# Performance work log

Hardware: AMD Instinct MI355X
Metric: run time of the kernel (lower is better)

Reference implementation:

```python
import jax, jax.numpy as jnp
import numpy as np

D_STATE = 16
D_CONV = 4
DT_RANK = 16  # ceil(d_model/16) = ceil(256/16)
N_LAYERS = 2
EPS = 1e-5


def _layernorm(x, g, b):
    m = jnp.mean(x, -1, keepdims=True)
    v = jnp.var(x, -1, keepdims=True)
    return (x - m) * jax.lax.rsqrt(v + EPS) * g + b


def _causal_conv(x, w, b):
    # x [B,L,D], depthwise causal conv, w [D,K], b [D]
    K = w.shape[1]
    L = x.shape[1]
    xp = jnp.pad(x, ((0, 0), (K - 1, 0), (0, 0)))
    y = sum(xp[:, k:k + L, :] * w[:, k] for k in range(K))
    return y + b


def _selective_scan(u, dt, A, Bm, Cm, D_skip):
    # u, dt [B,L,d]; A [d,n]; Bm, Cm [B,L,n]; D_skip [d]
    def step(h, inp):
        dt_t, B_t, C_t, u_t = inp  # [B,d],[B,n],[B,n],[B,d]
        dA = jnp.exp(dt_t[:, :, None] * A)                      # [B,d,n]
        h = dA * h + dt_t[:, :, None] * B_t[:, None, :] * u_t[:, :, None]
        y = jnp.einsum('bdn,bn->bd', h, C_t)
        return h, y

    Bsz, L, d = u.shape
    h0 = jnp.zeros((Bsz, d, A.shape[1]), u.dtype)
    xs = (dt.transpose(1, 0, 2), Bm.transpose(1, 0, 2),
          Cm.transpose(1, 0, 2), u.transpose(1, 0, 2))
    _, ys = jax.lax.scan(step, h0, xs)                          # [L,B,d]
    return ys.transpose(1, 0, 2) + u * D_skip


def _mamba_block(x, Wip, cw, cb, Wxp, Wdt, bdt, Alog, Dp, Wout):
    xz = x @ Wip                                                # [B,L,2*d_inner]
    d_inner = Wip.shape[1] // 2
    xc, z = xz[..., :d_inner], xz[..., d_inner:]
    xc = jax.nn.silu(_causal_conv(xc, cw, cb))
    xdbl = xc @ Wxp                                             # [B,L,dt_rank+2n]
    dt = jax.nn.softplus(xdbl[..., :DT_RANK] @ Wdt + bdt)
    Bm = xdbl[..., DT_RANK:DT_RANK + D_STATE]
    Cm = xdbl[..., DT_RANK + D_STATE:]
    A = -jnp.exp(Alog)
    y = _selective_scan(xc, dt, A, Bm, Cm, Dp)
    y = y * jax.nn.silu(z)
    return y @ Wout


def reference(z_t, W_in, b_in, ln_g, ln_b, W_inproj, conv_w, conv_b, W_xproj,
              W_dt, b_dt, A_log, D_skip, W_out, W_outp, b_outp, lno_g, lno_b):
    x = z_t @ W_in + b_in                                       # [B,L,d_model]
    for i in range(N_LAYERS):
        res = x
        xn = _layernorm(x, ln_g[i], ln_b[i])
        x = res + _mamba_block(xn, W_inproj[i], conv_w[i], conv_b[i],
                               W_xproj[i], W_dt[i], b_dt[i], A_log[i],
                               D_skip[i], W_out[i])  # dropout is identity in eval
    u = x @ W_outp + b_outp
    return _layernorm(u, lno_g, lno_b)


def setup_inputs() -> dict:
    key = jax.random.key(0)
    B, L = 16, 2048
    d_input, d_model, d_output, d_inner = 1088, 256, 64, 512
    n = N_LAYERS
    ks = jax.random.split(key, 10)

    def rn(k, shape, fan):
        return jax.random.normal(k, shape, jnp.float32) / np.float32(np.sqrt(fan))

    A_init = jnp.log(jnp.arange(1, D_STATE + 1, dtype=jnp.float32))
    return {
        'z_t': jax.random.normal(ks[0], (B, L, d_input), jnp.float32),
        'W_in': rn(ks[1], (d_input, d_model), d_input),
        'b_in': jnp.zeros((d_model,), jnp.float32),
        'ln_g': jnp.ones((n, d_model), jnp.float32),
        'ln_b': jnp.zeros((n, d_model), jnp.float32),
        'W_inproj': rn(ks[2], (n, d_model, 2 * d_inner), d_model),
        'conv_w': rn(ks[3], (n, d_inner, D_CONV), D_CONV),
        'conv_b': jnp.zeros((n, d_inner), jnp.float32),
        'W_xproj': rn(ks[4], (n, d_inner, DT_RANK + 2 * D_STATE), d_inner),
        'W_dt': rn(ks[5], (n, DT_RANK, d_inner), DT_RANK),
        'b_dt': jnp.full((n, d_inner), -4.6, jnp.float32),  # softplus ~ 0.01
        'A_log': jnp.broadcast_to(A_init, (n, d_inner, D_STATE)) + 0.0,
        'D_skip': jnp.ones((n, d_inner), jnp.float32),
        'W_out': rn(ks[6], (n, d_inner, d_model), d_inner),
        'W_outp': rn(ks[7], (d_model, d_output), d_model),
        'b_outp': jnp.zeros((d_output,), jnp.float32),
        'lno_g': jnp.ones((d_output,), jnp.float32),
        'lno_b': jnp.zeros((d_output,), jnp.float32),
    }
```

## Files before the change

kernel.cpp:

```cpp
#include <hip/hip_runtime.h>
#include <hip/hip_bf16.h>
#include <math.h>
#include <stdint.h>

#define L_SEQ 2048
#define BATCH 16
#define NROWS (BATCH * L_SEQ)
#define DMODEL 256
#define DINNER 512
#define C_CH 32
#define T_CH 64
#define LOG2E 1.4426950408889634f

typedef __attribute__((ext_vector_type(8))) __bf16 bf16x8;
typedef __attribute__((ext_vector_type(4))) float f32x4;
typedef __attribute__((ext_vector_type(8))) unsigned short u16x8;
typedef __attribute__((address_space(1))) const uint32_t gu32;
typedef __attribute__((address_space(3))) uint32_t lu32;

#if __has_builtin(__builtin_amdgcn_exp2f)
#define EXP2F __builtin_amdgcn_exp2f
#else
#define EXP2F exp2f
#endif

__device__ __forceinline__ float sigmoidf_(float x) { return 1.f / (1.f + __expf(-x)); }

__device__ __forceinline__ unsigned short f2bf(float f) {
    union { float f; uint32_t u; } v; v.f = f;
    uint32_t r = v.u + 0x7FFF + ((v.u >> 16) & 1);
    return (unsigned short)(r >> 16);
}
__device__ __forceinline__ float bf2f(unsigned short h) {
    union { uint32_t u; float f; } v; v.u = ((uint32_t)h) << 16;
    return v.f;
}

__device__ __forceinline__ void gld16(const void* g, void* l) {
    __builtin_amdgcn_global_load_lds((gu32*)g, (lu32*)l, 16, 0, 0);
}

template <int N> __device__ __forceinline__ void waitv() {
    if constexpr (N == 0)       asm volatile("s_waitcnt vmcnt(0)" ::: "memory");
    else if constexpr (N == 3)  asm volatile("s_waitcnt vmcnt(3)" ::: "memory");
    else if constexpr (N == 4)  asm volatile("s_waitcnt vmcnt(4)" ::: "memory");
    else if constexpr (N == 6)  asm volatile("s_waitcnt vmcnt(6)" ::: "memory");
    else if constexpr (N == 8)  asm volatile("s_waitcnt vmcnt(8)" ::: "memory");
    else if constexpr (N == 16) asm volatile("s_waitcnt vmcnt(16)" ::: "memory");
}

__global__ __launch_bounds__(256) void wtrans_all(
    const float* __restrict__ W_in, const float* __restrict__ W_inpr,
    const float* __restrict__ W_out, const float* __restrict__ W_xproj,
    const float* __restrict__ W_outp,
    unsigned short* __restrict__ WinT, unsigned short* __restrict__ WipT,
    unsigned short* __restrict__ WoutT, unsigned short* __restrict__ WxpT,
    unsigned short* __restrict__ WopT)
{
    const int bid = blockIdx.x, tid = threadIdx.x;
    if (bid < 1088) {
        int idx = bid * 256 + tid;
        int n = idx / 1088, k = idx % 1088;
        WinT[idx] = f2bf(W_in[(size_t)k * 256 + n]);
    } else if (bid < 3136) {
        int l = (bid - 1088) >> 10;
        int idx = ((bid - 1088) & 1023) * 256 + tid;
        int n = idx >> 8, k = idx & 255;
        WipT[(size_t)l * 262144 + idx] = f2bf(W_inpr[(size_t)l * 262144 + (size_t)k * 1024 + n]);
    } else if (bid < 4160) {
        int l = (bid - 3136) >> 9;
        int idx = ((bid - 3136) & 511) * 256 + tid;
        int n = idx >> 9, k = idx & 511;
        WoutT[(size_t)l * 131072 + idx] = f2bf(W_out[(size_t)l * 131072 + (size_t)k * 256 + n]);
    } else if (bid < 4672) {
        int l = (bid - 4160) >> 8;
        int idx = ((bid - 4160) & 255) * 256 + tid;
        int n = idx >> 9, k = idx & 511;
        WxpT[(size_t)l * 65536 + idx] =
            (n < 48) ? f2bf(W_xproj[(size_t)l * (512 * 48) + (size_t)k * 48 + n]) : (unsigned short)0;
    } else {
        int idx = (bid - 4672) * 256 + tid;
        int n = idx >> 8, k = idx & 255;
        WopT[idx] = (n < 64) ? f2bf(W_outp[(size_t)k * 64 + n]) : (unsigned short)0;
    }
}

template <int TM, int TN, int BK, bool A_F32, bool HAS_BIAS, bool HAS_RES, bool OUT_BF16, bool LN64OUT>
__global__ __launch_bounds__(256) void gemm_bf16(
    const void* __restrict__ Aptr, const unsigned short* __restrict__ Bt,
    const float* __restrict__ bias, const float* __restrict__ res,
    void* __restrict__ Cout, int M, int N, int K, int Nout,
    const float* __restrict__ lng, const float* __restrict__ lnb)
{
    constexpr int MR = TM / 32;
    constexpr int NR = TN / 32;
    constexpr int EWA = A_F32 ? 4 : 2;
    constexpr int RBA = BK * EWA;
    constexpr int RBB = BK * 2;
    constexpr int ABYTES = TM * RBA;
    constexpr int BBYTES = TN * RBB;
    constexpr int OPSA = ABYTES / 4096;
    constexpr int OPSB = BBYTES / 4096;
    constexpr int VOPS = OPSA + OPSB;
    constexpr bool SWZA = (RBA >= 128);
    constexpr bool SWZB = (RBB >= 128);
    constexpr int KK = BK / 32;
    __shared__ __align__(16) char Alds[2][ABYTES];
    __shared__ __align__(16) char Blds[2][BBYTES];
    const int tid = threadIdx.x;
    const int w = tid >> 6, lane = tid & 63;

    const int nwg = gridDim.x;
    const int q = nwg >> 3;
    const int wg = (blockIdx.x & 7) * q + (blockIdx.x >> 3);
    const int nx = N / TN;
    const int bm = (wg / nx) * TM, bn = (wg % nx) * TN;

    const int wr = (w >> 1) * (TM / 2), wc = (w & 1) * (TN / 2);
    const int fr = lane & 15, fq = lane >> 4;
    const size_t KbB = (size_t)K * 2;
    const size_t KbA = (size_t)K * EWA;

    const char* Ab = (const char*)Aptr;
    const char* Bb = (const char*)Bt;
    const int lds0 = w * 1024;

    f32x4 acc[MR][NR];
#pragma unroll
    for (int m = 0; m < MR; m++)
#pragma unroll
        for (int n = 0; n < NR; n++) acc[m][n] = (f32x4){0.f, 0.f, 0.f, 0.f};

    auto stageA = [&](int buf, int k0) {
        char* lA = Alds[buf];
#pragma unroll
        for (int i = 0; i < OPSA; i++) {
            const int o = i * 4096 + tid * 16;
            const int row = o / RBA;
            int col = o % RBA;
            if constexpr (SWZA) col ^= (row & 7) << 4;
            gld16(Ab + (size_t)(bm + row) * KbA + (size_t)k0 * EWA + col,
                  lA + i * 4096 + lds0);
        }
    };
    auto stageB = [&](int buf, int k0) {
        char* lB = Blds[buf];
#pragma unroll
        for (int i = 0; i < OPSB; i++) {
            const int o = i * 4096 + tid * 16;
            const int row = o / RBB;
            int col = o % RBB;
            if constexpr (SWZB) col ^= (row & 7) << 4;
            gld16(Bb + (size_t)(bn + row) * KbB + (size_t)k0 * 2 + col,
                  lB + i * 4096 + lds0);
        }
    };
    auto compute = [&](int buf) {
        const char* lA = Alds[buf];
        const char* lB = Blds[buf];
#pragma unroll
        for (int kk = 0; kk < KK; kk++) {
            bf16x8 af[MR], bg[NR];
#pragma unroll
            for (int m = 0; m < MR; m++) {
                const int row = wr + m * 16 + fr;
                const int sw = SWZA ? ((row & 7) << 4) : 0;
                if constexpr (A_F32) {
                    const int b0 = row * RBA + kk * 128 + fq * 32;
                    float4 x0 = *(const float4*)(lA + (b0 ^ sw));
                    float4 x1 = *(const float4*)(lA + ((b0 + 16) ^ sw));
                    bf16x8 a;
                    a[0]=(__bf16)x0.x; a[1]=(__bf16)x0.y; a[2]=(__bf16)x0.z; a[3]=(__bf16)x0.w;
                    a[4]=(__bf16)x1.x; a[5]=(__bf16)x1.y; a[6]=(__bf16)x1.z; a[7]=(__bf16)x1.w;
                    af[m] = a;
                } else {
                    const int c = kk * 64 + fq * 16;
                    af[m] = *(const bf16x8*)(lA + row * RBA + (c ^ sw));
                }
            }
#pragma unroll
            for (int n = 0; n < NR; n++) {
                const int row = wc + n * 16 + fr;
                const int sw = SWZB ? ((row & 7) << 4) : 0;
                const int c = kk * 64 + fq * 16;
                bg[n] = *(const bf16x8*)(lB + row * RBB + (c ^ sw));
            }
#pragma unroll
            for (int m = 0; m < MR; m++)
#pragma unroll
                for (int n = 0; n < NR; n++)
                    acc[m][n] = __builtin_amdgcn_mfma_f32_16x16x32_bf16(af[m], bg[n], acc[m][n], 0, 0, 0);
        }
    };

    const int NT = K / BK;

    stageA(0, 0); stageB(0, 0);
    asm volatile("s_waitcnt vmcnt(0) lgkmcnt(0)" ::: "memory");
    __builtin_amdgcn_s_barrier();
    __builtin_amdgcn_sched_barrier(0);

    for (int kt = 0; kt < NT; ++kt) {
        const int cur = kt & 1;
        const bool has_next = (kt + 1 < NT);
        if (has_next) {
            const int k0 = (kt + 1) * BK;
            stageA(cur ^ 1, k0); stageB(cur ^ 1, k0);
            waitv<VOPS>();
        } else {
            waitv<0>();
        }
        __builtin_amdgcn_s_barrier();
        __builtin_amdgcn_sched_barrier(0);

        compute(cur);

        asm volatile("s_waitcnt lgkmcnt(0)" ::: "memory");
        __builtin_amdgcn_s_barrier();
        __builtin_amdgcn_sched_barrier(0);
    }

    if constexpr (LN64OUT) {
        if (wc == 0) {
#pragma unroll
            for (int m = 0; m < MR; m++) {
#pragma unroll
                for (int r = 0; r < 4; r++) {
                    float v[NR]; float s = 0.f, sq = 0.f;
#pragma unroll
                    for (int n = 0; n < NR; n++) {
                        v[n] = acc[m][n][r] + bias[n * 16 + fr];
                        s += v[n]; sq += v[n] * v[n];
                    }
#pragma unroll
                    for (int off = 8; off; off >>= 1) { s += __shfl_xor(s, off); sq += __shfl_xor(sq, off); }
                    float mean = s * (1.f / 64.f);
                    float var = sq * (1.f / 64.f) - mean * mean;
                    float rs = rsqrtf(var + 1e-5f);
                    int row = bm + wr + m * 16 + fq * 4 + r;
#pragma unroll
                    for (int n = 0; n < NR; n++) {
                        int col = n * 16 + fr;
                        ((float*)Cout)[(size_t)row * 64 + col] = (v[n] - mean) * rs * lng[col] + lnb[col];
                    }
                }
            }
        }
    } else {
#pragma unroll
        for (int m = 0; m < MR; m++) {
#pragma unroll
            for (int n = 0; n < NR; n++) {
                int col = bn + wc + n * 16 + fr;
                if (col < Nout) {
#pragma unroll
                    for (int r = 0; r < 4; r++) {
                        int row = bm + wr + m * 16 + fq * 4 + r;
                        float v = acc[m][n][r];
                        if (HAS_BIAS) v += bias[col];
                        if (HAS_RES)  v += res[(size_t)row * Nout + col];
                        if (OUT_BF16) ((unsigned short*)Cout)[(size_t)row * Nout + col] = f2bf(v);
                        else          ((float*)Cout)[(size_t)row * Nout + col] = v;
                    }
                }
            }
        }
    }
}

__global__ __launch_bounds__(256) void ln256(
    const float* __restrict__ x, const float* __restrict__ g,
    const float* __restrict__ b, unsigned short* __restrict__ out)
{
    int lane = threadIdx.x & 63, wid = threadIdx.x >> 6;
    size_t r = (size_t)blockIdx.x * 4 + wid;
    const float4 v = *(const float4*)&x[r * 256 + lane * 4];
    float s = v.x + v.y + v.z + v.w;
    float sq = v.x * v.x + v.y * v.y + v.z * v.z + v.w * v.w;
#pragma unroll
    for (int off = 32; off; off >>= 1) { s += __shfl_xor(s, off); sq += __shfl_xor(sq, off); }
    float mean = s * (1.f / 256.f);
    float var = sq * (1.f / 256.f) - mean * mean;
    float rs = rsqrtf(var + 1e-5f);
    float4 gv = *(const float4*)&g[lane * 4];
    float4 bv = *(const float4*)&b[lane * 4];
    ushort4 o;
    o.x = f2bf((v.x - mean) * rs * gv.x + bv.x);
    o.y = f2bf((v.y - mean) * rs * gv.y + bv.y);
    o.z = f2bf((v.z - mean) * rs * gv.z + bv.z);
    o.w = f2bf((v.w - mean) * rs * gv.w + bv.w);
    *(ushort4*)&out[r * 256 + lane * 4] = o;
}

__global__ __launch_bounds__(256) void conv_silu8(
    const unsigned short* __restrict__ xz, const float* __restrict__ w,
    const float* __restrict__ cb, unsigned short* __restrict__ xc)
{
    int idx = blockIdx.x * 256 + threadIdx.x;
    int d8 = (idx & 63) << 3;
    int l  = (idx >> 6) & 2047;
    int b  = idx >> 17;
    const unsigned short* base = xz + ((size_t)b * L_SEQ + l) * 1024 + d8;
    u16x8 t0 = {0,0,0,0,0,0,0,0}, t1 = t0, t2 = t0;
    u16x8 t3 = *(const u16x8*)base;
    if (l >= 1) t2 = *(const u16x8*)(base - 1024);
    if (l >= 2) t1 = *(const u16x8*)(base - 2048);
    if (l >= 3) t0 = *(const u16x8*)(base - 3072);
    u16x8 o;
#pragma unroll
    for (int j = 0; j < 8; j++) {
        float4 wv = *(const float4*)&w[(d8 + j) * 4];
        float acc = cb[d8 + j];
        acc = fmaf(bf2f(t0[j]), wv.x, acc);
        acc = fmaf(bf2f(t1[j]), wv.y, acc);
        acc = fmaf(bf2f(t2[j]), wv.z, acc);
        acc = fmaf(bf2f(t3[j]), wv.w, acc);
        o[j] = f2bf(acc * sigmoidf_(acc));
    }
    *(u16x8*)&xc[((size_t)b * L_SEQ + l) * 512 + d8] = o;
}

__global__ __launch_bounds__(256) void scan_pass1(
    const unsigned short* __restrict__ xc, const float* __restrict__ xdbl,
    const float* __restrict__ Wdt, const float* __restrict__ bdt,
    const float* __restrict__ Alog,
    float* __restrict__ Tbuf, float* __restrict__ Sbuf)
{
    __shared__ float xs[T_CH][32];
    int idx = blockIdx.x * 256 + threadIdx.x;
    int d = idx & 511;
    int c = (idx >> 9) & (C_CH - 1);
    int b = idx >> 14;
    size_t r0 = (size_t)b * L_SEQ + (size_t)c * T_CH;
#pragma unroll
    for (int ii = 0; ii < 2; ii++) {
        int i = threadIdx.x + ii * 256, row = i >> 3, qq = i & 7;
        *(float4*)&xs[row][qq * 4] = *(const float4*)&xdbl[(r0 + row) * 48 + qq * 4];
    }
    __syncthreads();

    float wdt[16];
#pragma unroll
    for (int j = 0; j < 16; j++) wdt[j] = Wdt[j * 512 + d];
    const float bd = bdt[d];

    float a[16], a2[16], S[16];
#pragma unroll
    for (int n = 0; n < 16; n++) a[n] = -__expf(Alog[d * 16 + n]);
#pragma unroll
    for (int n = 0; n < 16; n++) a2[n] = a[n] * LOG2E;
#pragma unroll
    for (int n = 0; n < 16; n++) S[n] = 0.f;
    bool pow_ok = true;
#pragma unroll
    for (int n = 1; n < 16; n++)
        pow_ok = pow_ok && (fabsf(a[n] - (n + 1) * a[0]) <= 1e-3f * (n + 1) * fabsf(a[0]));
    const float a0l2 = a[0] * LOG2E;
    float Tsum = 0.f;

    if (pow_ok) {
        for (int t = 0; t < T_CH; t++) {
            float dtr = bd;
#pragma unroll
            for (int j = 0; j < 16; j++) dtr = fmaf(xs[t][j], wdt[j], dtr);
            float dtv = (dtr > 20.f) ? dtr : __logf(1.f + __expf(dtr));
            float u = bf2f(xc[(r0 + t) * 512 + d]);
            float dtu = dtv * u;
            Tsum += dtv;
            float e1 = EXP2F(dtv * a0l2), e2 = e1 * e1;
            S[0] = fmaf(e1, S[0], dtu * xs[t][16]);
            S[1] = fmaf(e2, S[1], dtu * xs[t][17]);
            float pm2 = e1, pm1 = e2;
#pragma unroll
            for (int n = 2; n < 16; n++) {
                float cur = pm2 * e2;
                S[n] = fmaf(cur, S[n], dtu * xs[t][16 + n]);
                pm2 = pm1; pm1 = cur;
            }
        }
    } else {
        for (int t = 0; t < T_CH; t++) {
            float dtr = bd;
#pragma unroll
            for (int j = 0; j < 16; j++) dtr = fmaf(xs[t][j], wdt[j], dtr);
            float dtv = (dtr > 20.f) ? dtr : __logf(1.f + __expf(dtr));
            float u = bf2f(xc[(r0 + t) * 512 + d]);
            float dtu = dtv * u;
            Tsum += dtv;
#pragma unroll
            for (int n = 0; n < 16; n++) {
                float dA = EXP2F(dtv * a2[n]);
                S[n] = fmaf(dA, S[n], dtu * xs[t][16 + n]);
            }
        }
    }
    Tbuf[idx] = Tsum;
    size_t o = (size_t)idx * 16;
#pragma unroll
    for (int qq = 0; qq < 4; qq++)
        *(float4*)&Sbuf[o + qq * 4] = make_float4(S[qq*4], S[qq*4+1], S[qq*4+2], S[qq*4+3]);
}

__global__ __launch_bounds__(256) void scan_pass2(
    const float* __restrict__ Tbuf, const float* __restrict__ Alog,
    float* __restrict__ Sbuf)
{
    int g = blockIdx.x * 256 + threadIdx.x;
    int nd = g & 8191;
    int b = g >> 13;
    int d = nd >> 4, n = nd & 15;
    const float a2 = -__expf(Alog[d * 16 + n]) * LOG2E;
    float H = 0.f;
    for (int c = 0; c < C_CH; c++) {
        size_t base = (size_t)(b * C_CH + c);
        float T = Tbuf[base * 512 + d];
        float P = EXP2F(T * a2);
        size_t idx = base * 8192 + nd;
        float S = Sbuf[idx];
        float Hn = fmaf(P, H, S);
        Sbuf[idx] = H;
        H = Hn;
    }
}

__global__ __launch_bounds__(256) void scan_pass3(
    const unsigned short* __restrict__ xcin, const unsigned short* __restrict__ xz,
    const float* __restrict__ xdbl, const float* __restrict__ Wdt,
    const float* __restrict__ bdt, const float* __restrict__ Alog,
    const float* __restrict__ Dsk, const float* __restrict__ Sbuf,
    unsigned short* __restrict__ y)
{
    __shared__ float xs[T_CH][48];
    int idx = blockIdx.x * 256 + threadIdx.x;
    int d = idx & 511;
    int c = (idx >> 9) & (C_CH - 1);
    int b = idx >> 14;
    size_t r0 = (size_t)b * L_SEQ + (size_t)c * T_CH;
#pragma unroll
    for (int ii = 0; ii < 3; ii++) {
        int i = threadIdx.x + ii * 256, row = i / 12, qq = i % 12;
        *(float4*)&xs[row][qq * 4] = *(const float4*)&xdbl[(r0 + row) * 48 + qq * 4];
    }
    __syncthreads();

    float wdt[16];
#pragma unroll
    for (int j = 0; j < 16; j++) wdt[j] = Wdt[j * 512 + d];
    const float bd = bdt[d];

    float a[16], a2[16], h[16];
#pragma unroll
    for (int n = 0; n < 16; n++) a[n] = -__expf(Alog[d * 16 + n]);
#pragma unroll
    for (int n = 0; n < 16; n++) a2[n] = a[n] * LOG2E;
    {
        size_t o = (size_t)idx * 16;
#pragma unroll
        for (int qq = 0; qq < 4; qq++) {
            float4 v = *(const float4*)&Sbuf[o + qq * 4];
            h[qq*4] = v.x; h[qq*4+1] = v.y; h[qq*4+2] = v.z; h[qq*4+3] = v.w;
        }
    }
    bool pow_ok = true;
#pragma unroll
    for (int n = 1; n < 16; n++)
        pow_ok = pow_ok && (fabsf(a[n] - (n + 1) * a[0]) <= 1e-3f * (n + 1) * fabsf(a[0]));
    const float a0l2 = a[0] * LOG2E;
    const float Dv = Dsk[d];

    if (pow_ok) {
        for (int t = 0; t < T_CH; t++) {
            size_t ridx = (r0 + t) * 512 + d;
            float dtr = bd;
#pragma unroll
            for (int j = 0; j < 16; j++) dtr = fmaf(xs[t][j], wdt[j], dtr);
            float dtv = (dtr > 20.f) ? dtr : __logf(1.f + __expf(dtr));
            float u = bf2f(xcin[ridx]);
            float dtu = dtv * u;
            float e1 = EXP2F(dtv * a0l2), e2 = e1 * e1;
            float yv = 0.f;
            h[0] = fmaf(e1, h[0], dtu * xs[t][16]);  yv = fmaf(h[0], xs[t][32], yv);
            h[1] = fmaf(e2, h[1], dtu * xs[t][17]);  yv = fmaf(h[1], xs[t][33], yv);
            float pm2 = e1, pm1 = e2;
#pragma unroll
            for (int n = 2; n < 16; n++) {
                float cur = pm2 * e2;
                h[n] = fmaf(cur, h[n], dtu * xs[t][16 + n]);
                yv = fmaf(h[n], xs[t][32 + n], yv);
                pm2 = pm1; pm1 = cur;
            }
            yv = fmaf(u, Dv, yv);
            float z = bf2f(xz[(r0 + t) * 1024 + 512 + d]);
            y[ridx] = f2bf(yv * z * sigmoidf_(z));
        }
    } else {
        for (int t = 0; t < T_CH; t++) {
            size_t ridx = (r0 + t) * 512 + d;
            float dtr = bd;
#pragma unroll
            for (int j = 0; j < 16; j++) dtr = fmaf(xs[t][j], wdt[j], dtr);
            float dtv = (dtr > 20.f) ? dtr : __logf(1.f + __expf(dtr));
            float u = bf2f(xcin[ridx]);
            float dtu = dtv * u;
            float yv = 0.f;
#pragma unroll
            for (int n = 0; n < 16; n++) {
                float dA = EXP2F(dtv * a2[n]);
                h[n] = fmaf(dA, h[n], dtu * xs[t][16 + n]);
                yv = fmaf(h[n], xs[t][32 + n], yv);
            }
            yv = fmaf(u, Dv, yv);
            float z = bf2f(xz[(r0 + t) * 1024 + 512 + d]);
            y[ridx] = f2bf(yv * z * sigmoidf_(z));
        }
    }
}

extern "C" void kernel_launch(void* const* d_in, const int* in_sizes, int n_in,
                              void* d_out, int out_size, void* d_ws, size_t ws_size,
                              hipStream_t stream)
{
    const float* z_t     = (const float*)d_in[0];
    const float* W_in    = (const float*)d_in[1];
    const float* b_in    = (const float*)d_in[2];
    const float* ln_g    = (const float*)d_in[3];
    const float* ln_b    = (const float*)d_in[4];
    const float* W_inpr  = (const float*)d_in[5];
    const float* conv_w  = (const float*)d_in[6];
    const float* conv_b  = (const float*)d_in[7];
    const float* W_xproj = (const float*)d_in[8];
    const float* W_dt    = (const float*)d_in[9];
    const float* b_dt    = (const float*)d_in[10];
    const float* A_log   = (const float*)d_in[11];
    const float* D_skip  = (const float*)d_in[12];
    const float* W_out   = (const float*)d_in[13];
    const float* W_outp  = (const float*)d_in[14];
    const float* b_outp  = (const float*)d_in[15];
    const float* lno_g   = (const float*)d_in[16];
    const float* lno_b   = (const float*)d_in[17];
    float* out           = (float*)d_out;

    char* p = (char*)d_ws;
    float*          x    = (float*)p;          p += (size_t)NROWS * DMODEL * 4;
    unsigned short* xn   = (unsigned short*)p; p += (size_t)NROWS * DMODEL * 2;
    unsigned short* xc   = (unsigned short*)p; p += (size_t)NROWS * DINNER * 2;
    unsigned short* xz   = (unsigned short*)p; p += (size_t)NROWS * 1024 * 2;
    float*          xdbl = (float*)p;          p += (size_t)NROWS * 48 * 4;
    float*          Pregion = (float*)p;       p += (size_t)BATCH * C_CH * DINNER * 16 * 4;
    float*          Sbuf = (float*)p;          p += (size_t)BATCH * C_CH * DINNER * 16 * 4;
    unsigned short* WinT  = (unsigned short*)p; p += (size_t)256 * 1088 * 2;
    unsigned short* WipT  = (unsigned short*)p; p += (size_t)2 * 1024 * 256 * 2;
    unsigned short* WoutT = (unsigned short*)p; p += (size_t)2 * 256 * 512 * 2;
    unsigned short* WxpT  = (unsigned short*)p; p += (size_t)2 * 128 * 512 * 2;
    unsigned short* WopT  = (unsigned short*)p; p += (size_t)128 * 256 * 2;
    float* Tbuf = Pregion;

    wtrans_all<<<4800, 256, 0, stream>>>(W_in, W_inpr, W_out, W_xproj, W_outp,
                                         WinT, WipT, WoutT, WxpT, WopT);

    gemm_bf16<64, 128, 64, true, true, false, false, false><<<(NROWS / 64) * (256 / 128), 256, 0, stream>>>(
        z_t, WinT, b_in, nullptr, x, NROWS, 256, 1088, 256, nullptr, nullptr);

    for (int layer = 0; layer < 2; ++layer) {
        ln256<<<NROWS / 4, 256, 0, stream>>>(x, ln_g + layer * 256, ln_b + layer * 256, xn);
        gemm_bf16<128, 128, 64, false, false, false, true, false><<<(NROWS / 128) * (1024 / 128), 256, 0, stream>>>(
            xn, WipT + (size_t)layer * 1024 * 256, nullptr, nullptr, xz, NROWS, 1024, 256, 1024, nullptr, nullptr);
        conv_silu8<<<NROWS * 64 / 256, 256, 0, stream>>>(
            xz, conv_w + layer * 512 * 4, conv_b + layer * 512, xc);
        gemm_bf16<64, 128, 64, false, false, false, false, false><<<(NROWS / 64) * (128 / 128), 256, 0, stream>>>(
            xc, WxpT + (size_t)layer * 128 * 512, nullptr, nullptr, xdbl, NROWS, 128, 512, 48, nullptr, nullptr);

        const float* Al_l  = A_log + layer * 512 * 16;
        const float* Wdt_l = W_dt + layer * 16 * 512;
        const float* bdt_l = b_dt + layer * 512;
        scan_pass1<<<BATCH * C_CH * DINNER / 256, 256, 0, stream>>>(
            xc, xdbl, Wdt_l, bdt_l, Al_l, Tbuf, Sbuf);
        scan_pass2<<<BATCH * DINNER * 16 / 256, 256, 0, stream>>>(Tbuf, Al_l, Sbuf);
        scan_pass3<<<BATCH * C_CH * DINNER / 256, 256, 0, stream>>>(
            xc, xz, xdbl, Wdt_l, bdt_l, Al_l, D_skip + layer * 512, Sbuf, xc);

        if (layer == 0) {
            gemm_bf16<64, 128, 64, false, false, true, false, false><<<(NROWS / 64) * (256 / 128), 256, 0, stream>>>(
                xc, WoutT, nullptr, x, x, NROWS, 256, 512, 256, nullptr, nullptr);
        } else {
            gemm_bf16<64, 128, 64, false, false, true, true, false><<<(NROWS / 64) * (256 / 128), 256, 0, stream>>>(
                xc, WoutT + (size_t)256 * 512, nullptr, x, xn, NROWS, 256, 512, 256, nullptr, nullptr);
        }
    }

    gemm_bf16<64, 128, 64, false, true, false, false, true><<<(NROWS / 64) * (128 / 128), 256, 0, stream>>>(
        xn, WopT, b_outp, nullptr, out, NROWS, 128, 256, 64, lno_g, lno_b);
}
```

Before: 526.6 us.

## Fuse LayerNorm into full-row GEMM epilogues for input and out projections

Removes the standalone ln256 kernel by widening the input-projection GEMM and the layer-0 output-projection GEMM to cover all 256 output columns per block (TN=256, BK=32). Their epilogues now compute per-row mean and variance through shuffles plus a cross-warp LDS reduction, then write both the fp32 residual and the bf16 normalized activations. This saves a full read of x and a separate launch per layer. In exchange, those GEMMs use different tiling with fewer blocks and a smaller K step, which may hurt occupancy or pipelining.

```diff
diff --git a/kernel.cpp b/kernel.cpp
--- a/kernel.cpp
+++ b/kernel.cpp
@@ -44,8 +44,10 @@
     if constexpr (N == 0)       asm volatile("s_waitcnt vmcnt(0)" ::: "memory");
     else if constexpr (N == 3)  asm volatile("s_waitcnt vmcnt(3)" ::: "memory");
     else if constexpr (N == 4)  asm volatile("s_waitcnt vmcnt(4)" ::: "memory");
+    else if constexpr (N == 5)  asm volatile("s_waitcnt vmcnt(5)" ::: "memory");
     else if constexpr (N == 6)  asm volatile("s_waitcnt vmcnt(6)" ::: "memory");
     else if constexpr (N == 8)  asm volatile("s_waitcnt vmcnt(8)" ::: "memory");
+    else if constexpr (N == 10) asm volatile("s_waitcnt vmcnt(10)" ::: "memory");
     else if constexpr (N == 16) asm volatile("s_waitcnt vmcnt(16)" ::: "memory");
 }
 
@@ -85,12 +87,14 @@
     }
 }
 
-template <int TM, int TN, int BK, bool A_F32, bool HAS_BIAS, bool HAS_RES, bool OUT_BF16, bool LN64OUT>
+template <int TM, int TN, int BK, bool A_F32, bool HAS_BIAS, bool HAS_RES,
+          bool OUT_BF16, bool LN64OUT, bool LN256OUT>
 __global__ __launch_bounds__(256) void gemm_bf16(
     const void* __restrict__ Aptr, const unsigned short* __restrict__ Bt,
     const float* __restrict__ bias, const float* __restrict__ res,
     void* __restrict__ Cout, int M, int N, int K, int Nout,
-    const float* __restrict__ lng, const float* __restrict__ lnb)
+    const float* __restrict__ lng, const float* __restrict__ lnb,
+    unsigned short* __restrict__ xnout)
 {
     constexpr int MR = TM / 32;
     constexpr int NR = TN / 32;
@@ -220,7 +224,67 @@
         __builtin_amdgcn_sched_barrier(0);
     }
 
-    if constexpr (LN64OUT) {
+    if constexpr (LN256OUT) {
+        float* xout = (float*)Cout;
+        float s_[MR][4], sq_[MR][4];
+#pragma unroll
+        for (int m = 0; m < MR; m++)
+#pragma unroll
+            for (int r = 0; r < 4; r++) { s_[m][r] = 0.f; sq_[m][r] = 0.f; }
+#pragma unroll
+        for (int m = 0; m < MR; m++) {
+#pragma unroll
+            for (int n = 0; n < NR; n++) {
+                const int col = wc + n * 16 + fr;
+#pragma unroll
+                for (int r = 0; r < 4; r++) {
+                    const int row = bm + wr + m * 16 + fq * 4 + r;
+                    float v = acc[m][n][r];
+                    if (HAS_BIAS) v += bias[col];
+                    if (HAS_RES)  v += res[(size_t)row * 256 + col];
+                    acc[m][n][r] = v;
+                    xout[(size_t)row * 256 + col] = v;
+                    s_[m][r] += v; sq_[m][r] += v * v;
+                }
+            }
+        }
+#pragma unroll
+        for (int m = 0; m < MR; m++)
+#pragma unroll
+            for (int r = 0; r < 4; r++)
+#pragma unroll
+                for (int off = 8; off; off >>= 1) {
+                    s_[m][r] += __shfl_xor(s_[m][r], off);
+                    sq_[m][r] += __shfl_xor(sq_[m][r], off);
+                }
+        float2* red = (float2*)&Alds[0][0];
+        if (fr == 0) {
+#pragma unroll
+            for (int m = 0; m < MR; m++)
+#pragma unroll
+                for (int r = 0; r < 4; r++)
+                    red[w * 32 + m * 16 + fq * 4 + r] = make_float2(s_[m][r], sq_[m][r]);
+        }
+        __syncthreads();
+#pragma unroll
+        for (int m = 0; m < MR; m++) {
+#pragma unroll
+            for (int r = 0; r < 4; r++) {
+                float2 o = red[(w ^ 1) * 32 + m * 16 + fq * 4 + r];
+                float s = s_[m][r] + o.x, sq = sq_[m][r] + o.y;
+                float mean = s * (1.f / 256.f);
+                float var = sq * (1.f / 256.f) - mean * mean;
+                float rs = rsqrtf(var + 1e-5f);
+                const int row = bm + wr + m * 16 + fq * 4 + r;
+#pragma unroll
+                for (int n = 0; n < NR; n++) {
+                    const int col = wc + n * 16 + fr;
+                    xnout[(size_t)row * 256 + col] =
+                        f2bf((acc[m][n][r] - mean) * rs * lng[col] + lnb[col]);
+                }
+            }
+        }
+    } else if constexpr (LN64OUT) {
         if (wc == 0) {
 #pragma unroll
             for (int m = 0; m < MR; m++) {
@@ -266,30 +330,6 @@
             }
         }
     }
-}
-
-__global__ __launch_bounds__(256) void ln256(
-    const float* __restrict__ x, const float* __restrict__ g,
-    const float* __restrict__ b, unsigned short* __restrict__ out)
-{
-    int lane = threadIdx.x & 63, wid = threadIdx.x >> 6;
-    size_t r = (size_t)blockIdx.x * 4 + wid;
-    const float4 v = *(const float4*)&x[r * 256 + lane * 4];
-    float s = v.x + v.y + v.z + v.w;
-    float sq = v.x * v.x + v.y * v.y + v.z * v.z + v.w * v.w;
-#pragma unroll
-    for (int off = 32; off; off >>= 1) { s += __shfl_xor(s, off); sq += __shfl_xor(sq, off); }
-    float mean = s * (1.f / 256.f);
-    float var = sq * (1.f / 256.f) - mean * mean;
-    float rs = rsqrtf(var + 1e-5f);
-    float4 gv = *(const float4*)&g[lane * 4];
-    float4 bv = *(const float4*)&b[lane * 4];
-    ushort4 o;
-    o.x = f2bf((v.x - mean) * rs * gv.x + bv.x);
-    o.y = f2bf((v.y - mean) * rs * gv.y + bv.y);
-    o.z = f2bf((v.z - mean) * rs * gv.z + bv.z);
-    o.w = f2bf((v.w - mean) * rs * gv.w + bv.w);
-    *(ushort4*)&out[r * 256 + lane * 4] = o;
 }
 
 __global__ __launch_bounds__(256) void conv_silu8(
@@ -558,17 +598,18 @@
     wtrans_all<<<4800, 256, 0, stream>>>(W_in, W_inpr, W_out, W_xproj, W_outp,
                                          WinT, WipT, WoutT, WxpT, WopT);
 
-    gemm_bf16<64, 128, 64, true, true, false, false, false><<<(NROWS / 64) * (256 / 128), 256, 0, stream>>>(
-        z_t, WinT, b_in, nullptr, x, NROWS, 256, 1088, 256, nullptr, nullptr);
+    gemm_bf16<64, 256, 32, true, true, false, false, false, true><<<NROWS / 64, 256, 0, stream>>>(
+        z_t, WinT, b_in, nullptr, x, NROWS, 256, 1088, 256, ln_g, ln_b, xn);
 
     for (int layer = 0; layer < 2; ++layer) {
-        ln256<<<NROWS / 4, 256, 0, stream>>>(x, ln_g + layer * 256, ln_b + layer * 256, xn);
-        gemm_bf16<128, 128, 64, false, false, false, true, false><<<(NROWS / 128) * (1024 / 128), 256, 0, stream>>>(
-            xn, WipT + (size_t)layer * 1024 * 256, nullptr, nullptr, xz, NROWS, 1024, 256, 1024, nullptr, nullptr);
+        gemm_bf16<128, 128, 64, false, false, false, true, false, false><<<(NROWS / 128) * (1024 / 128), 256, 0, stream>>>(
+            xn, WipT + (size_t)layer * 1024 * 256, nullptr, nullptr, xz, NROWS, 1024, 256, 1024,
+            nullptr, nullptr, nullptr);
         conv_silu8<<<NROWS * 64 / 256, 256, 0, stream>>>(
             xz, conv_w + layer * 512 * 4, conv_b + layer * 512, xc);
-        gemm_bf16<64, 128, 64, false, false, false, false, false><<<(NROWS / 64) * (128 / 128), 256, 0, stream>>>(
-            xc, WxpT + (size_t)layer * 128 * 512, nullptr, nullptr, xdbl, NROWS, 128, 512, 48, nullptr, nullptr);
+        gemm_bf16<64, 128, 64, false, false, false, false, false, false><<<(NROWS / 64) * (128 / 128), 256, 0, stream>>>(
+            xc, WxpT + (size_t)layer * 128 * 512, nullptr, nullptr, xdbl, NROWS, 128, 512, 48,
+            nullptr, nullptr, nullptr);
 
         const float* Al_l  = A_log + layer * 512 * 16;
         const float* Wdt_l = W_dt + layer * 16 * 512;
@@ -580,14 +621,15 @@
             xc, xz, xdbl, Wdt_l, bdt_l, Al_l, D_skip + layer * 512, Sbuf, xc);
 
         if (layer == 0) {
-            gemm_bf16<64, 128, 64, false, false, true, false, false><<<(NROWS / 64) * (256 / 128), 256, 0, stream>>>(
-                xc, WoutT, nullptr, x, x, NROWS, 256, 512, 256, nullptr, nullptr);
+            gemm_bf16<64, 256, 32, false, false, true, false, false, true><<<NROWS / 64, 256, 0, stream>>>(
+                xc, WoutT, nullptr, x, x, NROWS, 256, 512, 256, ln_g + 256, ln_b + 256, xn);
         } else {
-            gemm_bf16<64, 128, 64, false, false, true, true, false><<<(NROWS / 64) * (256 / 128), 256, 0, stream>>>(
-                xc, WoutT + (size_t)256 * 512, nullptr, x, xn, NROWS, 256, 512, 256, nullptr, nullptr);
-        }
-    }
-
-    gemm_bf16<64, 128, 64, false, true, false, false, true><<<(NROWS / 64) * (128 / 128), 256, 0, stream>>>(
-        xn, WopT, b_outp, nullptr, out, NROWS, 128, 256, 64, lno_g, lno_b);
-}
+            gemm_bf16<64, 128, 64, false, false, true, true, false, false><<<(NROWS / 64) * (256 / 128), 256, 0, stream>>>(
+                xc, WoutT + (size_t)256 * 512, nullptr, x, xn, NROWS, 256, 512, 256,
+                nullptr, nullptr, nullptr);
+        }
+    }
+
+    gemm_bf16<64, 128, 64, false, true, false, false, true, false><<<(NROWS / 64) * (128 / 128), 256, 0, stream>>>(
+        xn, WopT, b_outp, nullptr, out, NROWS, 128, 256, 64, lno_g, lno_b, nullptr);
+}
```

New measurement: 510.2 us, median of 2. 1.03x faster.
